# Performance work log

Measured on AMD Instinct MI355X. Metric: run time of the kernel, lower is better.

The kernel has to match this reference:

```python
import jax, jax.numpy as jnp
import numpy as np

HID = 3584; NH = 16; NKV = 8; HD = 256; S = 3072; WIN = 2048
SOFTCAP = 50.0; QSCALE = 256.0 ** -0.5  # query_pre_attn_scalar = 256
NEG = -2.3819763e38


def _rope(x, cos, sin):
    # x: (B, S, heads, HD); cos/sin: (S, HD//2). Gemma half-split complex RoPE.
    x1, x2 = jnp.split(x, 2, axis=-1)
    c = cos[None, :, None, :]
    s = sin[None, :, None, :]
    return jnp.concatenate([x1 * c - x2 * s, x1 * s + x2 * c], axis=-1)


def setup_inputs() -> dict:
    key = jax.random.key(0)
    k1, k2, k3 = jax.random.split(key, 3)
    hidden_states = jax.random.normal(k1, (1, S, HID), jnp.float32)
    qkv_w = jax.random.normal(k2, (NH * HD + 2 * NKV * HD, HID), jnp.float32) * 0.02
    o_w = jax.random.normal(k3, (HID, NH * HD), jnp.float32) * 0.02
    inv = 1.0 / (10000.0 ** (jnp.arange(0, HD, 2, dtype=jnp.float32) / HD))
    ang = jnp.arange(S, dtype=jnp.float32)[:, None] * inv[None, :]
    freqs_cis = jnp.stack([jnp.cos(ang), jnp.sin(ang)], axis=-1)  # (S, HD//2, 2)
    kv_write_indices = jnp.arange(S, dtype=jnp.int32)
    k_cache = jnp.zeros((1, S, NKV, HD), jnp.float32)
    v_cache = jnp.zeros((1, S, NKV, HD), jnp.float32)
    i = jnp.arange(S)[:, None]
    j = jnp.arange(S)[None, :]
    mask = jnp.where(j <= i, 0.0, NEG).astype(jnp.float32)[None, None]  # causal (1,1,S,S)
    return dict(hidden_states=hidden_states, freqs_cis=freqs_cis,
                kv_write_indices=kv_write_indices, k_cache=k_cache, v_cache=v_cache,
                mask=mask, qkv_w=qkv_w, o_w=o_w)


def reference(hidden_states, freqs_cis, kv_write_indices, k_cache, v_cache, mask, qkv_w, o_w):
    B, L, _ = hidden_states.shape
    qkv = hidden_states @ qkv_w.T  # (B, L, 8192)
    xq, xk, xv = jnp.split(qkv, [NH * HD, NH * HD + NKV * HD], axis=-1)
    xq = xq.reshape(B, L, NH, HD)
    xk = xk.reshape(B, L, NKV, HD)
    xv = xv.reshape(B, L, NKV, HD)
    cos, sin = freqs_cis[..., 0], freqs_cis[..., 1]
    xq = _rope(xq, cos, sin)
    xk = _rope(xk, cos, sin)
    # KV cache index_copy_ on dim 1
    k_all = k_cache.at[:, kv_write_indices].set(xk)  # (B, T, NKV, HD)
    v_all = v_cache.at[:, kv_write_indices].set(xv)
    T = k_all.shape[1]
    G = NH // NKV  # queries per kv head; grouped einsum avoids repeat_interleave
    q = (xq * QSCALE).transpose(0, 2, 1, 3).reshape(B, NKV, G, L, HD)
    k = k_all.transpose(0, 2, 1, 3)  # (B, NKV, T, HD)
    v = v_all.transpose(0, 2, 1, 3)
    scores = jnp.einsum('bkgsd,bktd->bkgst', q, k)
    # logit softcapping
    scores = jnp.tanh(scores / SOFTCAP) * SOFTCAP
    # sliding-window band applied on top of the provided (causal) mask
    i = jnp.arange(L)[:, None]
    j = jnp.arange(T)[None, :]
    band = (j >= i - WIN + 1) & (j <= i + WIN - 1)
    m = jnp.where(band, mask, NEG)  # (1,1,L,T)
    scores = scores + m[:, :, None]  # broadcast over group dim
    probs = jax.nn.softmax(scores.astype(jnp.float32), axis=-1).astype(q.dtype)
    out = jnp.einsum('bkgst,bktd->bkgsd', probs, v)
    out = out.reshape(B, NH, L, HD).transpose(0, 2, 1, 3).reshape(B, L, NH * HD)
    return out @ o_w.T
```

## Files before the change

### kernel.cpp

```cpp
#include <hip/hip_runtime.h>

#define S_LEN 3072
#define NHQ 16
#define NKVH 8
#define HDIM 256
#define WIN 2048
#define QKV_COLS 8192

typedef __bf16 bf16x8 __attribute__((ext_vector_type(8)));
typedef float f32x4 __attribute__((ext_vector_type(4)));
typedef float f32x16 __attribute__((ext_vector_type(16)));

__device__ __forceinline__ unsigned short f2bf(float f) {
    union { float f; unsigned u; } v; v.f = f;
    unsigned r = v.u + 0x7FFFu + ((v.u >> 16) & 1u);
    return (unsigned short)(r >> 16);
}
__device__ __forceinline__ float bf2f(unsigned short u) {
    union { unsigned u; float f; } v; v.u = ((unsigned)u) << 16; return v.f;
}

typedef __attribute__((address_space(3))) void lds_void_t;
typedef const __attribute__((address_space(1))) void glb_void_t;
__device__ __forceinline__ void async16(const void* g, void* l) {
    __builtin_amdgcn_global_load_lds((glb_void_t*)g, (lds_void_t*)l, 16, 0, 0);
}

__global__ __launch_bounds__(256) void cast_bf16_kernel(const float* __restrict__ src,
                                                        unsigned short* __restrict__ dst,
                                                        int n) {
    int i = (blockIdx.x * 256 + threadIdx.x) * 4;
    if (i >= n) return;
    float4 v = *(const float4*)(src + i);
    ushort4 o;
    o.x = f2bf(v.x); o.y = f2bf(v.y); o.z = f2bf(v.z); o.w = f2bf(v.w);
    *(ushort4*)(dst + i) = o;
}

template <int OUT_BF16>
__global__ __launch_bounds__(256) void gemm_bt(const unsigned short* __restrict__ A,
                                               const unsigned short* __restrict__ B,
                                               void* __restrict__ Cv,
                                               int N, int K) {
    __shared__ __align__(16) unsigned short At[128 * 32];
    __shared__ __align__(16) unsigned short Bt[128 * 32];
    const int tid = threadIdx.x;
    const int wid = tid >> 6, lane = tid & 63;
    const int ln = lane & 15, quad = lane >> 4;

    int bm, bn;
    {
        const int nwg = gridDim.x * gridDim.y;
        int orig = blockIdx.y * gridDim.x + blockIdx.x;
        int wg = orig;
        if ((nwg & 7) == 0) {
            const int cpx = nwg >> 3;
            wg = (orig & 7) * cpx + (orig >> 3);
        }
        bm = wg / gridDim.x;
        bn = wg % gridDim.x;
    }
    const int wm = wid >> 1, wn = wid & 1;

    const f32x4 fzero = {0.f, 0.f, 0.f, 0.f};
    f32x4 acc[4][4];
#pragma unroll
    for (int i = 0; i < 4; i++) {
#pragma unroll
        for (int j = 0; j < 4; j++) acc[i][j] = fzero;
    }

    const unsigned short* gA = A + (size_t)(bm * 128 + wid * 32 + (lane >> 2)) * K + (lane & 3) * 8;
    const unsigned short* gB = B + (size_t)(bn * 128 + wid * 32 + (lane >> 2)) * K + (lane & 3) * 8;
    unsigned short* lA = At + wid * 32 * 32;
    unsigned short* lB = Bt + wid * 32 * 32;

    for (int k0 = 0; k0 < K; k0 += 32) {
        async16(gA + k0, lA);
        async16(gA + k0 + 16 * K, lA + 16 * 32);
        async16(gB + k0, lB);
        async16(gB + k0 + 16 * K, lB + 16 * 32);
        __syncthreads();

        bf16x8 af[4], bfr[4];
#pragma unroll
        for (int mt = 0; mt < 4; mt++)
            af[mt] = *(const bf16x8*)(At + (wm * 64 + mt * 16 + ln) * 32 + quad * 8);
#pragma unroll
        for (int nt = 0; nt < 4; nt++)
            bfr[nt] = *(const bf16x8*)(Bt + (wn * 64 + nt * 16 + ln) * 32 + quad * 8);
#pragma unroll
        for (int mt = 0; mt < 4; mt++) {
#pragma unroll
            for (int nt = 0; nt < 4; nt++)
                acc[mt][nt] = __builtin_amdgcn_mfma_f32_16x16x32_bf16(af[mt], bfr[nt], acc[mt][nt], 0, 0, 0);
        }
        __syncthreads();
    }

    const int row0 = bm * 128 + wm * 64 + quad * 4;
    const int col0 = bn * 128 + wn * 64 + ln;
    if (OUT_BF16) {
        unsigned short* C = (unsigned short*)Cv;
#pragma unroll
        for (int mt = 0; mt < 4; mt++) {
#pragma unroll
            for (int nt = 0; nt < 4; nt++) {
#pragma unroll
                for (int rr = 0; rr < 4; rr++)
                    C[(size_t)(row0 + mt * 16 + rr) * N + col0 + nt * 16] = f2bf(acc[mt][nt][rr]);
            }
        }
    } else {
        float* C = (float*)Cv;
#pragma unroll
        for (int mt = 0; mt < 4; mt++) {
#pragma unroll
            for (int nt = 0; nt < 4; nt++) {
#pragma unroll
                for (int rr = 0; rr < 4; rr++)
                    C[(size_t)(row0 + mt * 16 + rr) * N + col0 + nt * 16] = acc[mt][nt][rr];
            }
        }
    }
}

__global__ __launch_bounds__(256) void rope_kernel(const unsigned short* __restrict__ qkv,
                                                   const float* __restrict__ freqs,
                                                   const int* __restrict__ kvidx,
                                                   unsigned short* __restrict__ Qb,
                                                   unsigned short* __restrict__ Kb) {
    int t = blockIdx.x * 256 + threadIdx.x;
    int d = t & 127;
    int t2 = t >> 7;
    int hh = t2 % 24;
    int pos = t2 / 24;
    if (pos >= S_LEN) return;
    float2 cs = *(const float2*)(freqs + ((size_t)pos * 128 + d) * 2);
    if (hh < NHQ) {
        const unsigned short* src = qkv + (size_t)pos * QKV_COLS + hh * HDIM + d;
        float x1 = bf2f(src[0]), x2 = bf2f(src[128]);
        float o1 = (x1 * cs.x - x2 * cs.y) * 0.0625f;
        float o2 = (x1 * cs.y + x2 * cs.x) * 0.0625f;
        unsigned short* dst = Qb + ((size_t)hh * S_LEN + pos) * HDIM + d;
        dst[0] = f2bf(o1);
        dst[128] = f2bf(o2);
    } else {
        int kvh = hh - NHQ;
        const unsigned short* src = qkv + (size_t)pos * QKV_COLS + NHQ * HDIM + kvh * HDIM + d;
        float x1 = bf2f(src[0]), x2 = bf2f(src[128]);
        float o1 = x1 * cs.x - x2 * cs.y;
        float o2 = x1 * cs.y + x2 * cs.x;
        int wpos = kvidx[pos];
        unsigned short* dst = Kb + ((size_t)kvh * S_LEN + wpos) * HDIM + d;
        dst[0] = f2bf(o1);
        dst[128] = f2bf(o2);
    }
}

__global__ __launch_bounds__(256) void vtrans_kernel(const unsigned short* __restrict__ qkv,
                                                     const int* __restrict__ kvidx,
                                                     unsigned short* __restrict__ Vbt) {
    __shared__ unsigned short T[64][72];
    int pos0 = blockIdx.x * 64;
    int c0 = blockIdx.y * 64;
    int a = threadIdx.x >> 6;
    int b = threadIdx.x & 63;
#pragma unroll
    for (int r = 0; r < 16; r++) {
        int pl = r * 4 + a;
        T[pl][b] = qkv[(size_t)(pos0 + pl) * QKV_COLS + 6144 + c0 + b];
    }
    __syncthreads();
    int wpos = kvidx[pos0 + b];
#pragma unroll
    for (int r = 0; r < 16; r++) {
        int cl = r * 4 + a;
        Vbt[(size_t)(c0 + cl) * S_LEN + wpos] = T[b][cl];
    }
}

__global__ __launch_bounds__(256, 1) void attn_kernel(const unsigned short* __restrict__ Qb,
                                                      const unsigned short* __restrict__ Kb,
                                                      const unsigned short* __restrict__ Vbt,
                                                      unsigned short* __restrict__ attn_out) {
    __shared__ __align__(16) unsigned short Kl[3][32 * 256];
    __shared__ __align__(16) unsigned short Vl[3][256 * 32];
    __shared__ __align__(16) unsigned short Plb[4][1024];

    const int h = blockIdx.x & 15;
    const int qb = 23 - (blockIdx.x >> 4);

    const int kv = h >> 1;
    const int q0 = qb * 128;
    const int tid = threadIdx.x;
    const int wid = tid >> 6, lane = tid & 63;
    const int ln32 = lane & 31, hi = lane >> 5;
    const int qw0 = q0 + wid * 32;

    bf16x8 qf[16];
    {
        const unsigned short* qrow = Qb + ((size_t)h * S_LEN + qw0 + ln32) * HDIM + hi * 8;
#pragma unroll
        for (int s = 0; s < 16; s++)
            qf[s] = *(const bf16x8*)(qrow + s * 16);
    }

    f32x16 pacc[8];
#pragma unroll
    for (int dt = 0; dt < 8; dt++) {
#pragma unroll
        for (int i = 0; i < 16; i++) pacc[dt][i] = 0.f;
    }
    float ps[16];
#pragma unroll
    for (int r = 0; r < 16; r++) ps[r] = 0.f;

    const int imin = qw0;
    const int imax = qw0 + 31;

    const int t_lo = (q0 >= WIN) ? ((q0 - (WIN - 1)) >> 5) : 0;
    const int t_hi = (q0 + 127) >> 5;
    const int ts = t_lo;
    const int te = t_hi + 1;

    const unsigned short* kSrcA = Kb + ((size_t)kv * S_LEN + (tid >> 5)) * HDIM
                                  + ((tid & 31) ^ ((tid >> 5) & 7)) * 8;
    const unsigned short* vSrcA = Vbt + ((size_t)kv * HDIM + (tid >> 2)) * S_LEN
                                  + ((tid & 3) ^ ((tid >> 3) & 3)) * 8;

    auto STAGE = [&](int tile, int b) {
        const int p0x = tile * 32;
        const unsigned short* ksg = kSrcA + (size_t)p0x * HDIM;
        const unsigned short* vsg = vSrcA + p0x;
#pragma unroll
        for (int c = 0; c < 4; c++)
            async16(ksg + (size_t)(c * 8) * HDIM, &Kl[b][(c * 256 + tid) * 8]);
#pragma unroll
        for (int c = 0; c < 4; c++)
            async16(vsg + (size_t)(c * 64) * S_LEN, &Vl[b][(c * 256 + tid) * 8]);
    };

    STAGE(ts, 0);
    STAGE(ts + 1, 1);

    unsigned short* plw = &Plb[wid][0];
    const int kswz = ln32 & 7;
    int rb = 0;

    for (int tt = ts; tt < te; tt++) {
        if (tt + 1 < te) { asm volatile("s_waitcnt vmcnt(8)" ::: "memory"); }
        else             { asm volatile("s_waitcnt vmcnt(0)" ::: "memory"); }
        __builtin_amdgcn_s_barrier();
        asm volatile("" ::: "memory");

        if (tt + 2 < te) {
            const int wb = (rb >= 1) ? rb - 1 : 2;
            STAGE(tt + 2, wb);
        }

        const int p0 = tt * 32;
        const bool live = (p0 <= imax) && (p0 + 31 >= imin - WIN + 1);
        if (live) {
            const unsigned short* kb = Kl[rb];
            f32x16 sacc;
#pragma unroll
            for (int i = 0; i < 16; i++) sacc[i] = 0.f;
#pragma unroll
            for (int s = 0; s < 16; s++) {
                bf16x8 kf = *(const bf16x8*)(kb + ln32 * 256 + ((((s << 1) + hi) ^ kswz) << 3));
                sacc = __builtin_amdgcn_mfma_f32_32x32x16_bf16(qf[s], kf, sacc, 0, 0, 0);
            }

            const bool full = (p0 + 31 <= imin) && (p0 >= imax - WIN + 1);
#pragma unroll
            for (int r = 0; r < 16; r++) {
                float z = __expf(sacc[r] * 0.04f);
                float t = fmaf(-100.f, __builtin_amdgcn_rcpf(z + 1.f), 50.f);
                float p = __expf(t);
                const int qloc = (r & 3) + 8 * (r >> 2) + 4 * hi;
                if (!full) {
                    const int i = qw0 + qloc;
                    const int j = p0 + ln32;
                    p = ((j <= i) && (j + WIN > i)) ? p : 0.f;
                }
                ps[r] += p;
                plw[qloc * 32 + (((ln32 >> 3) ^ ((qloc >> 1) & 3)) << 3) + (ln32 & 7)] = f2bf(p);
            }

            bf16x8 pa0 = *(const bf16x8*)(plw + ln32 * 32 + ((hi ^ ((ln32 >> 1) & 3)) << 3));
            bf16x8 pa1 = *(const bf16x8*)(plw + ln32 * 32 + (((2 + hi) ^ ((ln32 >> 1) & 3)) << 3));
            const unsigned short* vb = Vl[rb];
#pragma unroll
            for (int dt = 0; dt < 8; dt++) {
                const int d = dt * 32 + ln32;
                const int vswz = (d >> 1) & 3;
                bf16x8 v0 = *(const bf16x8*)(vb + d * 32 + ((hi ^ vswz) << 3));
                pacc[dt] = __builtin_amdgcn_mfma_f32_32x32x16_bf16(pa0, v0, pacc[dt], 0, 0, 0);
                bf16x8 v1 = *(const bf16x8*)(vb + d * 32 + (((2 + hi) ^ vswz) << 3));
                pacc[dt] = __builtin_amdgcn_mfma_f32_32x32x16_bf16(pa1, v1, pacc[dt], 0, 0, 0);
            }
        }
        rb = (rb >= 2) ? 0 : rb + 1;
    }

#pragma unroll
    for (int r = 0; r < 16; r++) {
        float s = ps[r];
#pragma unroll
        for (int o = 1; o <= 16; o <<= 1)
            s += __shfl_xor(s, o);
        ps[r] = s;
    }

#pragma unroll
    for (int dt = 0; dt < 8; dt++) {
#pragma unroll
        for (int r = 0; r < 16; r++) {
            const int q = qw0 + (r & 3) + 8 * (r >> 2) + 4 * hi;
            float o = pacc[dt][r] * __builtin_amdgcn_rcpf(ps[r]);
            attn_out[(size_t)q * 4096 + h * HDIM + dt * 32 + ln32] = f2bf(o);
        }
    }
}

extern "C" void kernel_launch(void* const* d_in, const int* in_sizes, int n_in,
                              void* d_out, int out_size, void* d_ws, size_t ws_size,
                              hipStream_t stream) {
    (void)in_sizes; (void)n_in; (void)out_size; (void)ws_size;
    const float* hidden = (const float*)d_in[0];
    const float* freqs  = (const float*)d_in[1];
    const int* kvidx    = (const int*)d_in[2];
    const float* qkv_w  = (const float*)d_in[6];
    const float* o_w    = (const float*)d_in[7];
    float* out = (float*)d_out;

    char* ws = (char*)d_ws;
    unsigned short* hs_bf   = (unsigned short*)(ws);
    unsigned short* w1_bf   = (unsigned short*)(ws + 22020096);
    unsigned short* w2_bf   = (unsigned short*)(ws + 80740352);
    unsigned short* qkv_bf  = (unsigned short*)(ws + 110100480);
    unsigned short* Qb      = (unsigned short*)(ws + 160432128);
    unsigned short* Kb      = (unsigned short*)(ws + 185597952);
    unsigned short* Vbt     = (unsigned short*)(ws + 198180864);
    unsigned short* attn_bf = (unsigned short*)(ws + 210763776);

    cast_bf16_kernel<<<10752, 256, 0, stream>>>(hidden, hs_bf, 11010048);
    cast_bf16_kernel<<<28672, 256, 0, stream>>>(qkv_w, w1_bf, 29360128);
    cast_bf16_kernel<<<14336, 256, 0, stream>>>(o_w, w2_bf, 14680064);

    gemm_bt<1><<<dim3(64, 24), 256, 0, stream>>>(hs_bf, w1_bf, (void*)qkv_bf, 8192, 3584);

    rope_kernel<<<36864, 256, 0, stream>>>(qkv_bf, freqs, kvidx, Qb, Kb);
    vtrans_kernel<<<dim3(48, 32), 256, 0, stream>>>(qkv_bf, kvidx, Vbt);

    attn_kernel<<<384, 256, 0, stream>>>(Qb, Kb, Vbt, attn_bf);

    gemm_bt<0><<<dim3(28, 24), 256, 0, stream>>>(attn_bf, w2_bf, (void*)out, 3584, 4096);
}
```

Baseline: 904.3 us.

## Triple-buffer GEMM LDS tiles with async prefetch two stages ahead

```diff
diff --git a/kernel.cpp b/kernel.cpp
--- a/kernel.cpp
+++ b/kernel.cpp
@@ -42,8 +42,8 @@
                                                const unsigned short* __restrict__ B,
                                                void* __restrict__ Cv,
                                                int N, int K) {
-    __shared__ __align__(16) unsigned short At[128 * 32];
-    __shared__ __align__(16) unsigned short Bt[128 * 32];
+    __shared__ __align__(16) unsigned short At[3][128 * 32];
+    __shared__ __align__(16) unsigned short Bt[3][128 * 32];
     const int tid = threadIdx.x;
     const int wid = tid >> 6, lane = tid & 63;
     const int ln = lane & 15, quad = lane >> 4;
@@ -72,30 +72,45 @@
 
     const unsigned short* gA = A + (size_t)(bm * 128 + wid * 32 + (lane >> 2)) * K + (lane & 3) * 8;
     const unsigned short* gB = B + (size_t)(bn * 128 + wid * 32 + (lane >> 2)) * K + (lane & 3) * 8;
-    unsigned short* lA = At + wid * 32 * 32;
-    unsigned short* lB = Bt + wid * 32 * 32;
-
-    for (int k0 = 0; k0 < K; k0 += 32) {
-        async16(gA + k0, lA);
-        async16(gA + k0 + 16 * K, lA + 16 * 32);
-        async16(gB + k0, lB);
-        async16(gB + k0 + 16 * K, lB + 16 * 32);
-        __syncthreads();
+    const int lbase = wid * 32 * 32;
+
+    auto STAGE = [&](int k0, int b) {
+        async16(gA + k0,          &At[b][lbase]);
+        async16(gA + k0 + 16 * K, &At[b][lbase + 16 * 32]);
+        async16(gB + k0,          &Bt[b][lbase]);
+        async16(gB + k0 + 16 * K, &Bt[b][lbase + 16 * 32]);
+    };
+
+    const int NT = K >> 5;
+    STAGE(0, 0);
+    STAGE(32, 1);
+    int rb = 0;
+
+    for (int t = 0; t < NT; ++t) {
+        if (t + 1 < NT) { asm volatile("s_waitcnt vmcnt(4)" ::: "memory"); }
+        else            { asm volatile("s_waitcnt vmcnt(0)" ::: "memory"); }
+        __builtin_amdgcn_s_barrier();
+        asm volatile("" ::: "memory");
+
+        if (t + 2 < NT) {
+            const int wb = (rb >= 1) ? rb - 1 : 2;
+            STAGE((t + 2) * 32, wb);
+        }
 
         bf16x8 af[4], bfr[4];
 #pragma unroll
         for (int mt = 0; mt < 4; mt++)
-            af[mt] = *(const bf16x8*)(At + (wm * 64 + mt * 16 + ln) * 32 + quad * 8);
+            af[mt] = *(const bf16x8*)(&At[rb][(wm * 64 + mt * 16 + ln) * 32 + quad * 8]);
 #pragma unroll
         for (int nt = 0; nt < 4; nt++)
-            bfr[nt] = *(const bf16x8*)(Bt + (wn * 64 + nt * 16 + ln) * 32 + quad * 8);
+            bfr[nt] = *(const bf16x8*)(&Bt[rb][(wn * 64 + nt * 16 + ln) * 32 + quad * 8]);
 #pragma unroll
         for (int mt = 0; mt < 4; mt++) {
 #pragma unroll
             for (int nt = 0; nt < 4; nt++)
                 acc[mt][nt] = __builtin_amdgcn_mfma_f32_16x16x32_bf16(af[mt], bfr[nt], acc[mt][nt], 0, 0, 0);
         }
-        __syncthreads();
+        rb = (rb >= 2) ? 0 : rb + 1;
     }
 
     const int row0 = bm * 128 + wm * 64 + quad * 4;
```

Result: faster. 874.4 us (-3.3%).
